# Kernel tuning notes

Measured on AMD Instinct MI355X. Metric: run time of the kernel, lower is better.

## Reference

```python
import jax, jax.numpy as jnp
import numpy as np

N_NODES = 50000
N_RAND_EDGES = 1_600_000
IN_FEATS = 512
HIDDEN = 256
NUM_CLASSES = 64


def setup_inputs() -> dict:
    key = jax.random.key(0)
    ks = jax.random.split(key, 6)
    src = jax.random.randint(ks[0], (N_RAND_EDGES,), 0, N_NODES, dtype=jnp.int32)
    dst = jax.random.randint(ks[1], (N_RAND_EDGES,), 0, N_NODES, dtype=jnp.int32)
    # dgl.add_self_loop(g): append (i, i) for every node
    loop = jnp.arange(N_NODES, dtype=jnp.int32)
    src = jnp.concatenate([src, loop])
    dst = jnp.concatenate([dst, loop])
    features = jax.random.normal(ks[2], (N_NODES, IN_FEATS), dtype=jnp.float32)
    W_conv = jax.random.normal(ks[3], (IN_FEATS, HIDDEN), dtype=jnp.float32) * (1.0 / np.sqrt(IN_FEATS))
    b_conv = jnp.zeros((HIDDEN,), dtype=jnp.float32)
    W2 = jax.random.normal(ks[4], (HIDDEN, NUM_CLASSES), dtype=jnp.float32) * (1.0 / np.sqrt(HIDDEN))
    b2 = jnp.zeros((NUM_CLASSES,), dtype=jnp.float32)
    return {"features": features, "W_conv": W_conv, "b_conv": b_conv,
            "W2": W2, "b2": b2, "src": src, "dst": dst}


def reference(features, W_conv, b_conv, W2, b2, src, dst):
    N = features.shape[0]
    ones = jnp.ones(src.shape[0], dtype=features.dtype)
    # symmetric ('both') normalization as in DGL GraphConv; self-loops guarantee deg >= 1
    deg_out = jax.ops.segment_sum(ones, src, num_segments=N)
    deg_in = jax.ops.segment_sum(ones, dst, num_segments=N)
    norm_src = jax.lax.rsqrt(deg_out)[:, None]  # [N, 1]
    norm_dst = jax.lax.rsqrt(deg_in)[:, None]
    # in_feats > hidden -> DGL multiplies by the weight before aggregating
    h = (features @ W_conv) * norm_src            # [N, H]
    agg = jax.ops.segment_sum(h[src], dst, num_segments=N)  # sparse SpMM: gather + scatter-add
    x = jax.nn.relu(agg * norm_dst + b_conv)      # [N, H]
    # dropout: identity in eval mode (deterministic reference)
    logits = x @ W2 + b2                          # [N, C]
    return jax.nn.log_softmax(logits, axis=1)
```

## Files before the change

kernel.cpp:

```cpp
#include <hip/hip_runtime.h>

typedef unsigned short u16;
typedef unsigned int u32;
typedef __attribute__((ext_vector_type(4))) float f32x4;
typedef __attribute__((ext_vector_type(8))) short s16x8;
typedef __attribute__((ext_vector_type(4))) unsigned short u16x4;
typedef __attribute__((ext_vector_type(8))) unsigned short u16x8;

#define IN_FEATS 512
#define HIDDEN   256
#define NCLS     64
#define NB       128
#define QBINS    12500
#define EPT      13

#define H8_CLIP  2.5f
#define H8_INV   (127.0f / H8_CLIP)
#define H8_SCALE (H8_CLIP / 127.0f)

static __device__ inline u16 f2bf(float f) {
    unsigned int u = __builtin_bit_cast(unsigned int, f);
    unsigned int r = (u + 0x7FFFu + ((u >> 16) & 1u)) >> 16;
    return (u16)r;
}


__launch_bounds__(1024)
__global__ void khist(const int* __restrict__ src, const int* __restrict__ dst,
                      u16* __restrict__ P, int E, int N) {
    __shared__ int bins[QBINS];
    const int b = blockIdx.x;
    const int t = threadIdx.x;
    const int lo = (int)((long)b * E / NB);
    const int hi = (int)((long)(b + 1) * E / NB);

    int se[EPT], de[EPT];
#pragma unroll
    for (int p = 0; p < EPT; p++) {
        int e = lo + t + p * 1024;
        se[p] = 0; de[p] = 0;
        if (e < hi) { se[p] = src[e]; de[p] = dst[e]; }
    }

#pragma unroll 1
    for (int q = 0; q < 4; q++) {
        const int base = q * QBINS;
        __syncthreads();
        for (int j = t; j < QBINS; j += 1024) bins[j] = 0;
        __syncthreads();
#pragma unroll
        for (int p = 0; p < EPT; p++) {
            int e = lo + t + p * 1024;
            if (e < hi) {
                unsigned rs = (unsigned)(se[p] - base), rd = (unsigned)(de[p] - base);
                if (rs < (unsigned)QBINS) atomicAdd(&bins[rs], 1);
                if (rd < (unsigned)QBINS) atomicAdd(&bins[rd], 0x10000);
            }
        }
        for (int e = lo + t + EPT * 1024; e < hi; e += 1024) {
            int s = src[e], d = dst[e];
            unsigned rs = (unsigned)(s - base), rd = (unsigned)(d - base);
            if (rs < (unsigned)QBINS) atomicAdd(&bins[rs], 1);
            if (rd < (unsigned)QBINS) atomicAdd(&bins[rd], 0x10000);
        }
        __syncthreads();
        for (int j = t; j < QBINS; j += 1024) {
            u32 v = (u32)bins[j];
            P[(size_t)b * 50000 + base + j] = (u16)((v & 0xffu) | ((v >> 8) & 0xff00u));
        }
    }
}

__launch_bounds__(256)
__global__ void kredscan(u16* __restrict__ P, int* __restrict__ rowptr,
                         int* __restrict__ bsum, float* __restrict__ ns,
                         float* __restrict__ nd, int N) {
    __shared__ int wsum[4];
    const int b = blockIdx.x, t = threadIdx.x;
    const int lane = t & 63, wave = t >> 6;
    const int j = b * 256 + t;
    u32 so = 0, si = 0;
    if (j < N) {
#pragma unroll 8
        for (int bb = 0; bb < NB; bb++) {
            u32 v = P[(size_t)bb * 50000 + j];
            P[(size_t)bb * 50000 + j] = (u16)si;
            so += v & 0xffu;
            si += v >> 8;
        }
        ns[j] = rsqrtf((float)so);
        nd[j] = rsqrtf((float)si);
    }
    int v = (j < N) ? (int)si : 0;
    int s = v;
#pragma unroll
    for (int off = 1; off < 64; off <<= 1) {
        int u = __shfl_up(s, off);
        if (lane >= off) s += u;
    }
    if (lane == 63) wsum[wave] = s;
    __syncthreads();
    int woff = 0;
#pragma unroll
    for (int w = 0; w < 4; w++) woff += (w < wave) ? wsum[w] : 0;
    if (j < N) rowptr[j] = woff + s - v;
    if (t == 255) bsum[b] = woff + s;
}

__launch_bounds__(256)
__global__ void kscanB(int* __restrict__ rowptr, const int* __restrict__ bsum,
                       int N, int nblk, int E) {
    __shared__ int wsum[4];
    const int b = blockIdx.x, t = threadIdx.x;
    const int lane = t & 63, wave = t >> 6;
    int v = (t < b && t < nblk) ? bsum[t] : 0;
#pragma unroll
    for (int off = 32; off; off >>= 1) v += __shfl_xor(v, off);
    if (lane == 0) wsum[wave] = v;
    __syncthreads();
    int offsum = wsum[0] + wsum[1] + wsum[2] + wsum[3];
    int j = b * 256 + t;
    if (j < N) rowptr[j] += offsum;
    if (b == 0 && t == 0) rowptr[N] = E;
}

__launch_bounds__(1024)
__global__ void kscat(const int* __restrict__ src, const int* __restrict__ dst,
                      const int* __restrict__ rowptr, const u16* __restrict__ P,
                      int* __restrict__ csc, int E, int N) {
    __shared__ int cur[QBINS];
    const int b = blockIdx.x;
    const int t = threadIdx.x;
    const int lo = (int)((long)b * E / NB);
    const int hi = (int)((long)(b + 1) * E / NB);

    int se[EPT], de[EPT];
#pragma unroll
    for (int p = 0; p < EPT; p++) {
        int e = lo + t + p * 1024;
        se[p] = 0; de[p] = 0;
        if (e < hi) { se[p] = src[e]; de[p] = dst[e]; }
    }

#pragma unroll 1
    for (int q = 0; q < 4; q++) {
        const int base = q * QBINS;
        __syncthreads();
        for (int j = t; j < QBINS; j += 1024) {
            int node = base + j;
            cur[j] = (node < N) ? rowptr[node] + (int)P[(size_t)b * 50000 + node] : 0;
        }
        __syncthreads();
#pragma unroll
        for (int p = 0; p < EPT; p++) {
            int e = lo + t + p * 1024;
            if (e < hi) {
                unsigned rd = (unsigned)(de[p] - base);
                if (rd < (unsigned)QBINS) {
                    int pos = atomicAdd(&cur[rd], 1);
                    csc[pos] = se[p] << 8;
                }
            }
        }
        for (int e = lo + t + EPT * 1024; e < hi; e += 1024) {
            int d = dst[e];
            unsigned rd = (unsigned)(d - base);
            if (rd < (unsigned)QBINS) {
                int pos = atomicAdd(&cur[rd], 1);
                csc[pos] = src[e] << 8;
            }
        }
    }
}

__global__ void kprep(const float* __restrict__ W, u16* __restrict__ Wt,
                      const float* __restrict__ W2, u16* __restrict__ W2t,
                      signed char* __restrict__ h8, int N) {
    int i = blockIdx.x * blockDim.x + threadIdx.x;
    if (i < IN_FEATS * HIDDEN) {
        int k = i >> 8, n = i & 255;
        Wt[n * IN_FEATS + k] = f2bf(W[i]);
    } else if (i < IN_FEATS * HIDDEN + HIDDEN * NCLS) {
        int ii = i - IN_FEATS * HIDDEN;
        int k = ii >> 6, n = ii & 63;
        W2t[n * HIDDEN + k] = f2bf(W2[ii]);
    } else if (i < IN_FEATS * HIDDEN + HIDDEN * NCLS + 64) {
        int ii = i - IN_FEATS * HIDDEN - HIDDEN * NCLS;
        ((int*)(h8 + (size_t)N * HIDDEN))[ii] = 0;
    }
}


static __device__ inline s16x8 ld_frag(const u16* p) {
    u16x4 lo = *(const u16x4*)p;
    u16x4 hi = *(const u16x4*)(p + 4);
    s16x8 r;
    r[0] = (short)lo.x; r[1] = (short)lo.y; r[2] = (short)lo.z; r[3] = (short)lo.w;
    r[4] = (short)hi.x; r[5] = (short)hi.y; r[6] = (short)hi.z; r[7] = (short)hi.w;
    return r;
}

__launch_bounds__(512)
__global__ void k_gemm1(const float* __restrict__ feat, const u16* __restrict__ Wt,
                        const float* __restrict__ norm_src, signed char* __restrict__ h8, int N) {
    __shared__ __align__(16) u16 At[128][40];
    const int t = threadIdx.x;
    const int lane = t & 63;
    const int wave = t >> 6;
    const int wm = wave & 1;
    const int wn = wave >> 1;
    const int m0 = blockIdx.x * 128;
    const int l15 = lane & 15;
    const int l4 = lane >> 4;

    f32x4 acc[4][4] = {};

    for (int kk = 0; kk < IN_FEATS; kk += 32) {
        __syncthreads();
#pragma unroll
        for (int rnd = 0; rnd < 2; rnd++) {
            int slot = t + rnd * 512;
            int r = slot >> 3, q = slot & 7;
            int gr = m0 + r;
            float4 v = make_float4(0.f, 0.f, 0.f, 0.f);
            if (gr < N) v = *(const float4*)&feat[(size_t)gr * IN_FEATS + kk + q * 4];
            u16x4 p;
            p.x = f2bf(v.x); p.y = f2bf(v.y); p.z = f2bf(v.z); p.w = f2bf(v.w);
            *(u16x4*)&At[r][q * 4] = p;
        }
        __syncthreads();

        s16x8 a[4], b[4];
#pragma unroll
        for (int ni = 0; ni < 4; ni++)
            b[ni] = ld_frag(&Wt[(size_t)(wn * 64 + ni * 16 + l15) * IN_FEATS + kk + l4 * 8]);
#pragma unroll
        for (int mi = 0; mi < 4; mi++) a[mi] = ld_frag(&At[wm * 64 + mi * 16 + l15][l4 * 8]);
#pragma unroll
        for (int mi = 0; mi < 4; mi++)
#pragma unroll
            for (int ni = 0; ni < 4; ni++)
                acc[mi][ni] = __builtin_amdgcn_mfma_f32_16x16x32_bf16(a[mi], b[ni], acc[mi][ni], 0, 0, 0);
    }

#pragma unroll
    for (int mi = 0; mi < 4; mi++) {
#pragma unroll
        for (int q = 0; q < 4; q++) {
            int row = m0 + wm * 64 + mi * 16 + l4 * 4 + q;
            if (row < N) {
                float nsv = norm_src[row] * H8_INV;
#pragma unroll
                for (int ni = 0; ni < 4; ni++) {
                    int col = wn * 64 + ni * 16 + l15;
                    int v = (int)rintf(acc[mi][ni][q] * nsv);
                    v = max(-127, min(127, v));
                    h8[(size_t)row * HIDDEN + col] = (signed char)v;
                }
            }
        }
    }
}

__launch_bounds__(256)
__global__ void k_spmm(const signed char* __restrict__ h8, const int* __restrict__ rowptr,
                       const int* __restrict__ csc, const float* __restrict__ nd,
                       const float* __restrict__ bconv, u16* __restrict__ x, int N) {
    const int t = threadIdx.x;
    const int lane = t & 63;
    const int half = lane >> 5;
    const int hl = lane & 31;
    const int ZOFF = N * HIDDEN;
    const int gw = (blockIdx.x * blockDim.x + t) >> 6;
    const int nw = (gridDim.x * blockDim.x) >> 6;
    const int npair = (N + 1) >> 1;

    for (int pair = gw; pair < npair; pair += nw) {
        int node = pair * 2 + half;
        bool valid = node < N;
        int start = 0, deg = 0;
        if (valid) { start = rowptr[node]; deg = rowptr[node + 1] - start; }
        int maxdeg = max(deg, __shfl_xor(deg, 32));
        int a0 = 0, a1 = 0, a2 = 0, a3 = 0, a4 = 0, a5 = 0, a6 = 0, a7 = 0;

        for (int base = 0; base < maxdeg; base += 32) {
            int ev = ZOFF;
            if (base + hl < deg) ev = csc[start + base + hl];
            int cntmax = min(32, maxdeg - base);
            int i = 0;
            for (; i + 4 <= cntmax; i += 4) {
                int sb = (half << 5) + i;
                int o0 = __shfl(ev, sb);
                int o1 = __shfl(ev, sb + 1);
                int o2 = __shfl(ev, sb + 2);
                int o3 = __shfl(ev, sb + 3);
                int2 w0 = *(const int2*)&h8[o0 + hl * 8];
                int2 w1 = *(const int2*)&h8[o1 + hl * 8];
                int2 w2 = *(const int2*)&h8[o2 + hl * 8];
                int2 w3 = *(const int2*)&h8[o3 + hl * 8];
                a0 += ((w0.x << 24) >> 24) + ((w1.x << 24) >> 24) + ((w2.x << 24) >> 24) + ((w3.x << 24) >> 24);
                a1 += ((w0.x << 16) >> 24) + ((w1.x << 16) >> 24) + ((w2.x << 16) >> 24) + ((w3.x << 16) >> 24);
                a2 += ((w0.x << 8) >> 24) + ((w1.x << 8) >> 24) + ((w2.x << 8) >> 24) + ((w3.x << 8) >> 24);
                a3 += (w0.x >> 24) + (w1.x >> 24) + (w2.x >> 24) + (w3.x >> 24);
                a4 += ((w0.y << 24) >> 24) + ((w1.y << 24) >> 24) + ((w2.y << 24) >> 24) + ((w3.y << 24) >> 24);
                a5 += ((w0.y << 16) >> 24) + ((w1.y << 16) >> 24) + ((w2.y << 16) >> 24) + ((w3.y << 16) >> 24);
                a6 += ((w0.y << 8) >> 24) + ((w1.y << 8) >> 24) + ((w2.y << 8) >> 24) + ((w3.y << 8) >> 24);
                a7 += (w0.y >> 24) + (w1.y >> 24) + (w2.y >> 24) + (w3.y >> 24);
            }
            for (; i < cntmax; i++) {
                int o = __shfl(ev, (half << 5) + i);
                int2 w = *(const int2*)&h8[o + hl * 8];
                a0 += (w.x << 24) >> 24;
                a1 += (w.x << 16) >> 24;
                a2 += (w.x << 8) >> 24;
                a3 += w.x >> 24;
                a4 += (w.y << 24) >> 24;
                a5 += (w.y << 16) >> 24;
                a6 += (w.y << 8) >> 24;
                a7 += w.y >> 24;
            }
        }

        if (valid) {
            float scnd = nd[node] * H8_SCALE;
            float4 ba = *(const float4*)&bconv[hl * 8];
            float4 bb = *(const float4*)&bconv[hl * 8 + 4];
            u16x8 o;
            o[0] = f2bf(fmaxf((float)a0 * scnd + ba.x, 0.f));
            o[1] = f2bf(fmaxf((float)a1 * scnd + ba.y, 0.f));
            o[2] = f2bf(fmaxf((float)a2 * scnd + ba.z, 0.f));
            o[3] = f2bf(fmaxf((float)a3 * scnd + ba.w, 0.f));
            o[4] = f2bf(fmaxf((float)a4 * scnd + bb.x, 0.f));
            o[5] = f2bf(fmaxf((float)a5 * scnd + bb.y, 0.f));
            o[6] = f2bf(fmaxf((float)a6 * scnd + bb.z, 0.f));
            o[7] = f2bf(fmaxf((float)a7 * scnd + bb.w, 0.f));
            *(u16x8*)&x[(size_t)node * HIDDEN + hl * 8] = o;
        }
    }
}

__launch_bounds__(256)
__global__ void k_gemm2(const u16* __restrict__ x, const u16* __restrict__ W2t,
                        const float* __restrict__ b2, float* __restrict__ out, int N) {
    __shared__ __align__(16) u16 Bs[NCLS][HIDDEN + 8];
    const int t = threadIdx.x;
    for (int i = t; i < NCLS * HIDDEN / 8; i += 256) {
        int idx = i * 8;
        int n = idx >> 8, k = idx & 255;
        *(u16x8*)&Bs[n][k] = *(const u16x8*)&W2t[n * HIDDEN + k];
    }
    __syncthreads();

    const int lane = t & 63;
    const int wave = t >> 6;
    const int l15 = lane & 15;
    const int l4 = lane >> 4;
    const int r0 = blockIdx.x * 128 + wave * 32;

    float bb[4];
#pragma unroll
    for (int ni = 0; ni < 4; ni++) bb[ni] = b2[ni * 16 + l15];

    f32x4 acc[2][4] = {};
#pragma unroll
    for (int kk = 0; kk < HIDDEN; kk += 32) {
        s16x8 b[4];
#pragma unroll
        for (int ni = 0; ni < 4; ni++) b[ni] = ld_frag(&Bs[ni * 16 + l15][kk + l4 * 8]);
#pragma unroll
        for (int mi = 0; mi < 2; mi++) {
            int row = r0 + mi * 16 + l15;
            s16x8 a = {};
            if (row < N) a = ld_frag(&x[(size_t)row * HIDDEN + kk + l4 * 8]);
#pragma unroll
            for (int ni = 0; ni < 4; ni++)
                acc[mi][ni] = __builtin_amdgcn_mfma_f32_16x16x32_bf16(a, b[ni], acc[mi][ni], 0, 0, 0);
        }
    }

#pragma unroll
    for (int mi = 0; mi < 2; mi++) {
#pragma unroll
        for (int q = 0; q < 4; q++) {
            int row = r0 + mi * 16 + l4 * 4 + q;
            float v0 = acc[mi][0][q] + bb[0];
            float v1 = acc[mi][1][q] + bb[1];
            float v2 = acc[mi][2][q] + bb[2];
            float v3 = acc[mi][3][q] + bb[3];
            float m = fmaxf(fmaxf(v0, v1), fmaxf(v2, v3));
#pragma unroll
            for (int off = 1; off < 16; off <<= 1) m = fmaxf(m, __shfl_xor(m, off));
            float s = __expf(v0 - m) + __expf(v1 - m) + __expf(v2 - m) + __expf(v3 - m);
#pragma unroll
            for (int off = 1; off < 16; off <<= 1) s += __shfl_xor(s, off);
            float lg = m + __logf(s);
            if (row < N) {
                out[(size_t)row * NCLS + 0 * 16 + l15] = v0 - lg;
                out[(size_t)row * NCLS + 1 * 16 + l15] = v1 - lg;
                out[(size_t)row * NCLS + 2 * 16 + l15] = v2 - lg;
                out[(size_t)row * NCLS + 3 * 16 + l15] = v3 - lg;
            }
        }
    }
}


extern "C" void kernel_launch(void* const* d_in, const int* in_sizes, int n_in,
                              void* d_out, int out_size, void* d_ws, size_t ws_size,
                              hipStream_t stream) {
    const float* feat = (const float*)d_in[0];
    const float* Wc   = (const float*)d_in[1];
    const float* bc   = (const float*)d_in[2];
    const float* W2   = (const float*)d_in[3];
    const float* b2   = (const float*)d_in[4];
    const int*   src  = (const int*)d_in[5];
    const int*   dst  = (const int*)d_in[6];
    const int N = in_sizes[0] / IN_FEATS;
    const int E = in_sizes[5];
    float* out = (float*)d_out;

    char* ws = (char*)d_ws;
    size_t off = 0;
    auto alloc = [&](size_t b) {
        char* p = ws + off;
        off = (off + b + 255) & ~(size_t)255;
        return p;
    };
    signed char* h8 = (signed char*)alloc((size_t)(N + 1) * HIDDEN);
    u16* x      = (u16*)alloc((size_t)N * HIDDEN * 2);
    u16* Wt     = (u16*)alloc((size_t)IN_FEATS * HIDDEN * 2);
    u16* W2t    = (u16*)alloc((size_t)HIDDEN * NCLS * 2);
    int* rowptr = (int*)alloc((size_t)(N + 1) * 4);
    int* bsum   = (int*)alloc((size_t)256 * 4);
    float* ns   = (float*)alloc((size_t)N * 4);
    float* nd   = (float*)alloc((size_t)N * 4);
    int* csc    = (int*)alloc((size_t)E * 4);
    u16* P      = (u16*)alloc((size_t)NB * 50000 * 2);

    const int nblk = (N + 255) / 256;
    const int nprep = (IN_FEATS * HIDDEN + HIDDEN * NCLS + 64 + 255) / 256;

    khist<<<dim3(NB), dim3(1024), 0, stream>>>(src, dst, P, E, N);
    kredscan<<<dim3(nblk), dim3(256), 0, stream>>>(P, rowptr, bsum, ns, nd, N);
    kscanB<<<dim3(nblk), dim3(256), 0, stream>>>(rowptr, bsum, N, nblk, E);
    kscat<<<dim3(NB), dim3(1024), 0, stream>>>(src, dst, rowptr, P, csc, E, N);
    kprep<<<dim3(nprep), dim3(256), 0, stream>>>(Wc, Wt, W2, W2t, h8, N);
    k_gemm1<<<dim3((N + 127) / 128), dim3(512), 0, stream>>>(feat, Wt, ns, h8, N);
    k_spmm<<<dim3(2048), dim3(256), 0, stream>>>(h8, rowptr, csc, nd, bc, x, N);
    k_gemm2<<<dim3((N + 127) / 128), dim3(256), 0, stream>>>(x, W2t, b2, out, N);
}
```

Baseline: 180.9 us.

## Sort CSC by source band and stage W tile in LDS for gemm1

The histogram now keeps per-destination counts split into four source-node bands packed as bytes. The scatter runs in four passes, one per band, so each CSC segment is roughly ordered by source. This should improve gather locality in the SpMM at the cost of 16 scatter passes instead of 4 and a larger partial-count buffer. Separately, gemm1 loads the weight tile cooperatively into shared memory instead of having each wave read fragments from global memory.

```diff
diff --git a/kernel.cpp b/kernel.cpp
--- a/kernel.cpp
+++ b/kernel.cpp
@@ -1,5 +1,6 @@
 #include <hip/hip_runtime.h>
 
+typedef unsigned char u8;
 typedef unsigned short u16;
 typedef unsigned int u32;
 typedef __attribute__((ext_vector_type(4))) float f32x4;
@@ -27,8 +28,9 @@
 
 __launch_bounds__(1024)
 __global__ void khist(const int* __restrict__ src, const int* __restrict__ dst,
-                      u16* __restrict__ P, int E, int N) {
+                      u8* __restrict__ Pout, u32* __restrict__ Pband, int E, int N) {
     __shared__ int bins[QBINS];
+    __shared__ u32 binb[QBINS];
     const int b = blockIdx.x;
     const int t = threadIdx.x;
     const int lo = (int)((long)b * E / NB);
@@ -46,7 +48,7 @@
     for (int q = 0; q < 4; q++) {
         const int base = q * QBINS;
         __syncthreads();
-        for (int j = t; j < QBINS; j += 1024) bins[j] = 0;
+        for (int j = t; j < QBINS; j += 1024) { bins[j] = 0; binb[j] = 0; }
         __syncthreads();
 #pragma unroll
         for (int p = 0; p < EPT; p++) {
@@ -54,42 +56,55 @@
             if (e < hi) {
                 unsigned rs = (unsigned)(se[p] - base), rd = (unsigned)(de[p] - base);
                 if (rs < (unsigned)QBINS) atomicAdd(&bins[rs], 1);
-                if (rd < (unsigned)QBINS) atomicAdd(&bins[rd], 0x10000);
+                if (rd < (unsigned)QBINS) {
+                    int sb = (unsigned)se[p] / QBINS;
+                    atomicAdd(&binb[rd], 1u << (sb * 8));
+                }
             }
         }
         for (int e = lo + t + EPT * 1024; e < hi; e += 1024) {
             int s = src[e], d = dst[e];
             unsigned rs = (unsigned)(s - base), rd = (unsigned)(d - base);
             if (rs < (unsigned)QBINS) atomicAdd(&bins[rs], 1);
-            if (rd < (unsigned)QBINS) atomicAdd(&bins[rd], 0x10000);
+            if (rd < (unsigned)QBINS) {
+                int sb = (unsigned)s / QBINS;
+                atomicAdd(&binb[rd], 1u << (sb * 8));
+            }
         }
         __syncthreads();
         for (int j = t; j < QBINS; j += 1024) {
-            u32 v = (u32)bins[j];
-            P[(size_t)b * 50000 + base + j] = (u16)((v & 0xffu) | ((v >> 8) & 0xff00u));
+            Pout[(size_t)b * 50000 + base + j] = (u8)bins[j];
+            Pband[(size_t)b * 50000 + base + j] = binb[j];
         }
     }
 }
 
 __launch_bounds__(256)
-__global__ void kredscan(u16* __restrict__ P, int* __restrict__ rowptr,
-                         int* __restrict__ bsum, float* __restrict__ ns,
-                         float* __restrict__ nd, int N) {
+__global__ void kredscan(const u8* __restrict__ Pout, u32* __restrict__ Pband,
+                         int* __restrict__ rowptr, int* __restrict__ bsum,
+                         float* __restrict__ ns, float* __restrict__ nd, int N) {
     __shared__ int wsum[4];
     const int b = blockIdx.x, t = threadIdx.x;
     const int lane = t & 63, wave = t >> 6;
     const int j = b * 256 + t;
-    u32 so = 0, si = 0;
+    u32 si = 0;
     if (j < N) {
+        u32 so = 0, Tp = 0;
 #pragma unroll 8
         for (int bb = 0; bb < NB; bb++) {
-            u32 v = P[(size_t)bb * 50000 + j];
-            P[(size_t)bb * 50000 + j] = (u16)si;
-            so += v & 0xffu;
-            si += v >> 8;
-        }
+            so += Pout[(size_t)bb * 50000 + j];
+            Tp += Pband[(size_t)bb * 50000 + j];
+        }
+        si = (Tp & 0xffu) + ((Tp >> 8) & 0xffu) + ((Tp >> 16) & 0xffu) + (Tp >> 24);
         ns[j] = rsqrtf((float)so);
         nd[j] = rsqrtf((float)si);
+        u32 run = (Tp << 8) + (Tp << 16) + (Tp << 24);
+#pragma unroll 8
+        for (int bb = 0; bb < NB; bb++) {
+            u32 vb = Pband[(size_t)bb * 50000 + j];
+            Pband[(size_t)bb * 50000 + j] = run;
+            run += vb;
+        }
     }
     int v = (j < N) ? (int)si : 0;
     int s = v;
@@ -126,7 +141,7 @@
 
 __launch_bounds__(1024)
 __global__ void kscat(const int* __restrict__ src, const int* __restrict__ dst,
-                      const int* __restrict__ rowptr, const u16* __restrict__ P,
+                      const int* __restrict__ rowptr, const u32* __restrict__ Pband,
                       int* __restrict__ csc, int E, int N) {
     __shared__ int cur[QBINS];
     const int b = blockIdx.x;
@@ -134,40 +149,49 @@
     const int lo = (int)((long)b * E / NB);
     const int hi = (int)((long)(b + 1) * E / NB);
 
-    int se[EPT], de[EPT];
+    int se[EPT], de[EPT], sv[EPT];
 #pragma unroll
     for (int p = 0; p < EPT; p++) {
         int e = lo + t + p * 1024;
-        se[p] = 0; de[p] = 0;
-        if (e < hi) { se[p] = src[e]; de[p] = dst[e]; }
+        se[p] = 0; de[p] = 0; sv[p] = 0;
+        if (e < hi) {
+            se[p] = src[e]; de[p] = dst[e];
+            sv[p] = (unsigned)se[p] / QBINS;
+        }
     }
 
 #pragma unroll 1
-    for (int q = 0; q < 4; q++) {
-        const int base = q * QBINS;
-        __syncthreads();
-        for (int j = t; j < QBINS; j += 1024) {
-            int node = base + j;
-            cur[j] = (node < N) ? rowptr[node] + (int)P[(size_t)b * 50000 + node] : 0;
-        }
-        __syncthreads();
-#pragma unroll
-        for (int p = 0; p < EPT; p++) {
-            int e = lo + t + p * 1024;
-            if (e < hi) {
-                unsigned rd = (unsigned)(de[p] - base);
+    for (int sb = 0; sb < 4; sb++) {
+#pragma unroll 1
+        for (int q = 0; q < 4; q++) {
+            const int base = q * QBINS;
+            __syncthreads();
+            for (int j = t; j < QBINS; j += 1024) {
+                int node = base + j;
+                cur[j] = (node < N)
+                    ? rowptr[node] + (int)((Pband[(size_t)b * 50000 + node] >> (sb * 8)) & 0xffu)
+                    : 0;
+            }
+            __syncthreads();
+#pragma unroll
+            for (int p = 0; p < EPT; p++) {
+                int e = lo + t + p * 1024;
+                if (e < hi && sv[p] == sb) {
+                    unsigned rd = (unsigned)(de[p] - base);
+                    if (rd < (unsigned)QBINS) {
+                        int pos = atomicAdd(&cur[rd], 1);
+                        csc[pos] = se[p] << 8;
+                    }
+                }
+            }
+            for (int e = lo + t + EPT * 1024; e < hi; e += 1024) {
+                int s = src[e], d = dst[e];
+                if ((int)((unsigned)s / QBINS) != sb) continue;
+                unsigned rd = (unsigned)(d - base);
                 if (rd < (unsigned)QBINS) {
                     int pos = atomicAdd(&cur[rd], 1);
-                    csc[pos] = se[p] << 8;
+                    csc[pos] = s << 8;
                 }
-            }
-        }
-        for (int e = lo + t + EPT * 1024; e < hi; e += 1024) {
-            int d = dst[e];
-            unsigned rd = (unsigned)(d - base);
-            if (rd < (unsigned)QBINS) {
-                int pos = atomicAdd(&cur[rd], 1);
-                csc[pos] = src[e] << 8;
             }
         }
     }
@@ -204,6 +228,7 @@
 __global__ void k_gemm1(const float* __restrict__ feat, const u16* __restrict__ Wt,
                         const float* __restrict__ norm_src, signed char* __restrict__ h8, int N) {
     __shared__ __align__(16) u16 At[128][40];
+    __shared__ __align__(16) u16 Bt[256][40];
     const int t = threadIdx.x;
     const int lane = t & 63;
     const int wave = t >> 6;
@@ -228,14 +253,22 @@
             p.x = f2bf(v.x); p.y = f2bf(v.y); p.z = f2bf(v.z); p.w = f2bf(v.w);
             *(u16x4*)&At[r][q * 4] = p;
         }
+#pragma unroll
+        for (int rnd = 0; rnd < 2; rnd++) {
+            int slot = t + rnd * 512;
+            int r = slot >> 2, q = slot & 3;
+            u16x4 w0 = *(const u16x4*)&Wt[(size_t)r * IN_FEATS + kk + q * 8];
+            u16x4 w1 = *(const u16x4*)&Wt[(size_t)r * IN_FEATS + kk + q * 8 + 4];
+            *(u16x4*)&Bt[r][q * 8] = w0;
+            *(u16x4*)&Bt[r][q * 8 + 4] = w1;
+        }
         __syncthreads();
 
         s16x8 a[4], b[4];
 #pragma unroll
-        for (int ni = 0; ni < 4; ni++)
-            b[ni] = ld_frag(&Wt[(size_t)(wn * 64 + ni * 16 + l15) * IN_FEATS + kk + l4 * 8]);
-#pragma unroll
         for (int mi = 0; mi < 4; mi++) a[mi] = ld_frag(&At[wm * 64 + mi * 16 + l15][l4 * 8]);
+#pragma unroll
+        for (int ni = 0; ni < 4; ni++) b[ni] = ld_frag(&Bt[wn * 64 + ni * 16 + l15][l4 * 8]);
 #pragma unroll
         for (int mi = 0; mi < 4; mi++)
 #pragma unroll
@@ -435,15 +468,16 @@
     float* ns   = (float*)alloc((size_t)N * 4);
     float* nd   = (float*)alloc((size_t)N * 4);
     int* csc    = (int*)alloc((size_t)E * 4);
-    u16* P      = (u16*)alloc((size_t)NB * 50000 * 2);
+    u8*  Pout   = (u8*)alloc((size_t)NB * 50000);
+    u32* Pband  = (u32*)alloc((size_t)NB * 50000 * 4);
 
     const int nblk = (N + 255) / 256;
     const int nprep = (IN_FEATS * HIDDEN + HIDDEN * NCLS + 64 + 255) / 256;
 
-    khist<<<dim3(NB), dim3(1024), 0, stream>>>(src, dst, P, E, N);
-    kredscan<<<dim3(nblk), dim3(256), 0, stream>>>(P, rowptr, bsum, ns, nd, N);
+    khist<<<dim3(NB), dim3(1024), 0, stream>>>(src, dst, Pout, Pband, E, N);
+    kredscan<<<dim3(nblk), dim3(256), 0, stream>>>(Pout, Pband, rowptr, bsum, ns, nd, N);
     kscanB<<<dim3(nblk), dim3(256), 0, stream>>>(rowptr, bsum, N, nblk, E);
-    kscat<<<dim3(NB), dim3(1024), 0, stream>>>(src, dst, rowptr, P, csc, E, N);
+    kscat<<<dim3(NB), dim3(1024), 0, stream>>>(src, dst, rowptr, Pband, csc, E, N);
     kprep<<<dim3(nprep), dim3(256), 0, stream>>>(Wc, Wt, W2, W2t, h8, N);
     k_gemm1<<<dim3((N + 127) / 128), dim3(512), 0, stream>>>(feat, Wt, ns, h8, N);
     k_spmm<<<dim3(2048), dim3(256), 0, stream>>>(h8, rowptr, csc, nd, bc, x, N);
```

After: 252.0 us. 39.3% more time.

## Halve histogram passes with packed 16-bit bins; pipeline GEMM1 with LDS-staged weights

Applied to the files above, without the earlier changes.

The degree histogram and CSC scatter kernels now use 256 blocks with two node-range passes instead of four. Counts are packed two per 32-bit LDS word so a half-range fits in shared memory. GEMM1 switches to 64-row tiles with 256 threads, stages both the feature tile and the weight tile in LDS, and prefetches the next K slice into registers while the current slice is computed. This aims to cut repeated edge scans and the global-memory weight fragment loads, at the cost of more LDS per block and a larger partial-count array P to reduce. Per-block 8-bit counts are less likely to overflow because each block now covers fewer edges.

```diff
diff --git a/kernel.cpp b/kernel.cpp
--- a/kernel.cpp
+++ b/kernel.cpp
@@ -1,5 +1,6 @@
 #include <hip/hip_runtime.h>
 
+typedef unsigned char u8;
 typedef unsigned short u16;
 typedef unsigned int u32;
 typedef __attribute__((ext_vector_type(4))) float f32x4;
@@ -10,9 +11,9 @@
 #define IN_FEATS 512
 #define HIDDEN   256
 #define NCLS     64
-#define NB       128
-#define QBINS    12500
-#define EPT      13
+#define NB       256
+#define HBINS    25000
+#define EPT      7
 
 #define H8_CLIP  2.5f
 #define H8_INV   (127.0f / H8_CLIP)
@@ -28,7 +29,7 @@
 __launch_bounds__(1024)
 __global__ void khist(const int* __restrict__ src, const int* __restrict__ dst,
                       u16* __restrict__ P, int E, int N) {
-    __shared__ int bins[QBINS];
+    __shared__ u32 pk[25000];
     const int b = blockIdx.x;
     const int t = threadIdx.x;
     const int lo = (int)((long)b * E / NB);
@@ -43,30 +44,31 @@
     }
 
 #pragma unroll 1
-    for (int q = 0; q < 4; q++) {
-        const int base = q * QBINS;
-        __syncthreads();
-        for (int j = t; j < QBINS; j += 1024) bins[j] = 0;
+    for (int half = 0; half < 2; half++) {
+        const int base = half * HBINS;
+        __syncthreads();
+        for (int j = t; j < 25000; j += 1024) pk[j] = 0;
         __syncthreads();
 #pragma unroll
         for (int p = 0; p < EPT; p++) {
             int e = lo + t + p * 1024;
             if (e < hi) {
                 unsigned rs = (unsigned)(se[p] - base), rd = (unsigned)(de[p] - base);
-                if (rs < (unsigned)QBINS) atomicAdd(&bins[rs], 1);
-                if (rd < (unsigned)QBINS) atomicAdd(&bins[rd], 0x10000);
+                if (rs < (unsigned)HBINS) atomicAdd(&pk[rs >> 1], 1u << ((rs & 1) << 4));
+                if (rd < (unsigned)HBINS) atomicAdd(&pk[12500 + (rd >> 1)], 1u << ((rd & 1) << 4));
             }
         }
         for (int e = lo + t + EPT * 1024; e < hi; e += 1024) {
             int s = src[e], d = dst[e];
             unsigned rs = (unsigned)(s - base), rd = (unsigned)(d - base);
-            if (rs < (unsigned)QBINS) atomicAdd(&bins[rs], 1);
-            if (rd < (unsigned)QBINS) atomicAdd(&bins[rd], 0x10000);
-        }
-        __syncthreads();
-        for (int j = t; j < QBINS; j += 1024) {
-            u32 v = (u32)bins[j];
-            P[(size_t)b * 50000 + base + j] = (u16)((v & 0xffu) | ((v >> 8) & 0xff00u));
+            if (rs < (unsigned)HBINS) atomicAdd(&pk[rs >> 1], 1u << ((rs & 1) << 4));
+            if (rd < (unsigned)HBINS) atomicAdd(&pk[12500 + (rd >> 1)], 1u << ((rd & 1) << 4));
+        }
+        __syncthreads();
+        for (int j = t; j < HBINS; j += 1024) {
+            u32 o  = (pk[j >> 1] >> ((j & 1) << 4)) & 0xffffu;
+            u32 in = (pk[12500 + (j >> 1)] >> ((j & 1) << 4)) & 0xffffu;
+            P[(size_t)b * 50000 + base + j] = (u16)((o & 0xffu) | ((in & 0xffu) << 8));
         }
     }
 }
@@ -79,8 +81,9 @@
     const int b = blockIdx.x, t = threadIdx.x;
     const int lane = t & 63, wave = t >> 6;
     const int j = b * 256 + t;
-    u32 so = 0, si = 0;
+    u32 si = 0;
     if (j < N) {
+        u32 so = 0;
 #pragma unroll 8
         for (int bb = 0; bb < NB; bb++) {
             u32 v = P[(size_t)bb * 50000 + j];
@@ -128,7 +131,7 @@
 __global__ void kscat(const int* __restrict__ src, const int* __restrict__ dst,
                       const int* __restrict__ rowptr, const u16* __restrict__ P,
                       int* __restrict__ csc, int E, int N) {
-    __shared__ int cur[QBINS];
+    __shared__ int cur[HBINS];
     const int b = blockIdx.x;
     const int t = threadIdx.x;
     const int lo = (int)((long)b * E / NB);
@@ -143,10 +146,10 @@
     }
 
 #pragma unroll 1
-    for (int q = 0; q < 4; q++) {
-        const int base = q * QBINS;
-        __syncthreads();
-        for (int j = t; j < QBINS; j += 1024) {
+    for (int half = 0; half < 2; half++) {
+        const int base = half * HBINS;
+        __syncthreads();
+        for (int j = t; j < HBINS; j += 1024) {
             int node = base + j;
             cur[j] = (node < N) ? rowptr[node] + (int)P[(size_t)b * 50000 + node] : 0;
         }
@@ -156,7 +159,7 @@
             int e = lo + t + p * 1024;
             if (e < hi) {
                 unsigned rd = (unsigned)(de[p] - base);
-                if (rd < (unsigned)QBINS) {
+                if (rd < (unsigned)HBINS) {
                     int pos = atomicAdd(&cur[rd], 1);
                     csc[pos] = se[p] << 8;
                 }
@@ -165,7 +168,7 @@
         for (int e = lo + t + EPT * 1024; e < hi; e += 1024) {
             int d = dst[e];
             unsigned rd = (unsigned)(d - base);
-            if (rd < (unsigned)QBINS) {
+            if (rd < (unsigned)HBINS) {
                 int pos = atomicAdd(&cur[rd], 1);
                 csc[pos] = src[e] << 8;
             }
@@ -200,42 +203,71 @@
     return r;
 }
 
-__launch_bounds__(512)
+__launch_bounds__(256)
 __global__ void k_gemm1(const float* __restrict__ feat, const u16* __restrict__ Wt,
                         const float* __restrict__ norm_src, signed char* __restrict__ h8, int N) {
-    __shared__ __align__(16) u16 At[128][40];
+    __shared__ __align__(16) u16 At[64][40];
+    __shared__ __align__(16) u16 Bt[256][40];
     const int t = threadIdx.x;
     const int lane = t & 63;
-    const int wave = t >> 6;
-    const int wm = wave & 1;
-    const int wn = wave >> 1;
-    const int m0 = blockIdx.x * 128;
+    const int wn = t >> 6;
+    const int m0 = blockIdx.x * 64;
     const int l15 = lane & 15;
     const int l4 = lane >> 4;
 
-    f32x4 acc[4][4] = {};
-
-    for (int kk = 0; kk < IN_FEATS; kk += 32) {
-        __syncthreads();
+    float4 pa[2];
+    u16x4 pb[4][2];
+
+    auto LOAD = [&](int kk) {
 #pragma unroll
         for (int rnd = 0; rnd < 2; rnd++) {
-            int slot = t + rnd * 512;
+            int slot = t + rnd * 256;
             int r = slot >> 3, q = slot & 7;
             int gr = m0 + r;
-            float4 v = make_float4(0.f, 0.f, 0.f, 0.f);
-            if (gr < N) v = *(const float4*)&feat[(size_t)gr * IN_FEATS + kk + q * 4];
+            pa[rnd] = (gr < N) ? *(const float4*)&feat[(size_t)gr * IN_FEATS + kk + q * 4]
+                               : make_float4(0.f, 0.f, 0.f, 0.f);
+        }
+#pragma unroll
+        for (int rnd = 0; rnd < 4; rnd++) {
+            int slot = t + rnd * 256;
+            int r = slot >> 2, q = slot & 3;
+            pb[rnd][0] = *(const u16x4*)&Wt[(size_t)r * IN_FEATS + kk + q * 8];
+            pb[rnd][1] = *(const u16x4*)&Wt[(size_t)r * IN_FEATS + kk + q * 8 + 4];
+        }
+    };
+    auto STORE = [&]() {
+#pragma unroll
+        for (int rnd = 0; rnd < 2; rnd++) {
+            int slot = t + rnd * 256;
+            int r = slot >> 3, q = slot & 7;
             u16x4 p;
-            p.x = f2bf(v.x); p.y = f2bf(v.y); p.z = f2bf(v.z); p.w = f2bf(v.w);
+            p.x = f2bf(pa[rnd].x); p.y = f2bf(pa[rnd].y);
+            p.z = f2bf(pa[rnd].z); p.w = f2bf(pa[rnd].w);
             *(u16x4*)&At[r][q * 4] = p;
         }
+#pragma unroll
+        for (int rnd = 0; rnd < 4; rnd++) {
+            int slot = t + rnd * 256;
+            int r = slot >> 2, q = slot & 3;
+            *(u16x4*)&Bt[r][q * 8] = pb[rnd][0];
+            *(u16x4*)&Bt[r][q * 8 + 4] = pb[rnd][1];
+        }
+    };
+
+    f32x4 acc[4][4] = {};
+    LOAD(0);
+
+    for (int kk = 0; kk < IN_FEATS; kk += 32) {
+        __syncthreads();
+        STORE();
+        if (kk + 32 < IN_FEATS) LOAD(kk + 32);
         __syncthreads();
 
         s16x8 a[4], b[4];
 #pragma unroll
-        for (int ni = 0; ni < 4; ni++)
-            b[ni] = ld_frag(&Wt[(size_t)(wn * 64 + ni * 16 + l15) * IN_FEATS + kk + l4 * 8]);
-#pragma unroll
-        for (int mi = 0; mi < 4; mi++) a[mi] = ld_frag(&At[wm * 64 + mi * 16 + l15][l4 * 8]);
+        for (int mi = 0; mi < 4; mi++) a[mi] = ld_frag(&At[mi * 16 + l15][l4 * 8]);
+#pragma unroll
+        for (int ni = 0; ni < 4; ni++) b[ni] = ld_frag(&Bt[wn * 64 + ni * 16 + l15][l4 * 8]);
 #pragma unroll
         for (int mi = 0; mi < 4; mi++)
 #pragma unroll
@@ -247,7 +279,7 @@
     for (int mi = 0; mi < 4; mi++) {
 #pragma unroll
         for (int q = 0; q < 4; q++) {
-            int row = m0 + wm * 64 + mi * 16 + l4 * 4 + q;
+            int row = m0 + mi * 16 + l4 * 4 + q;
             if (row < N) {
                 float nsv = norm_src[row] * H8_INV;
 #pragma unroll
@@ -445,7 +477,7 @@
     kscanB<<<dim3(nblk), dim3(256), 0, stream>>>(rowptr, bsum, N, nblk, E);
     kscat<<<dim3(NB), dim3(1024), 0, stream>>>(src, dst, rowptr, P, csc, E, N);
     kprep<<<dim3(nprep), dim3(256), 0, stream>>>(Wc, Wt, W2, W2t, h8, N);
-    k_gemm1<<<dim3((N + 127) / 128), dim3(512), 0, stream>>>(feat, Wt, ns, h8, N);
+    k_gemm1<<<dim3((N + 63) / 64), dim3(256), 0, stream>>>(feat, Wt, ns, h8, N);
     k_spmm<<<dim3(2048), dim3(256), 0, stream>>>(h8, rowptr, csc, nd, bc, x, N);
     k_gemm2<<<dim3((N + 127) / 128), dim3(256), 0, stream>>>(x, W2t, b2, out, N);
 }
```

Result: faster. 172.5 us (-4.6%).
